# Performance work log

Hardware: AMD Instinct MI355X
Metric: run time of the kernel (lower is better)

Reference implementation:

```python
import jax, jax.numpy as jnp
import numpy as np

N, D, E, C = 8192, 64, 524288, 2


def setup_inputs() -> dict:
    key = jax.random.key(0)
    ks = jax.random.split(key, 14)
    src = jax.random.randint(ks[0], (E,), 0, N, dtype=jnp.int32)
    dst = jax.random.randint(ks[1], (E,), 0, N, dtype=jnp.int32)
    h = jax.random.normal(ks[2], (N, D), jnp.float32)
    # dense adjacency consistent with the edge list (A[u,v]=1 for edge u->v)
    one = jnp.ones((E,), jnp.float32)
    A = jnp.zeros((N, N), jnp.float32).at[src, dst].max(one)
    # motif adjacencies: random subsets of the base edges
    keep1 = jax.random.bernoulli(ks[3], 0.5, (E,)).astype(jnp.float32)
    keep2 = jax.random.bernoulli(ks[4], 0.3, (E,)).astype(jnp.float32)
    A1 = jnp.zeros((N, N), jnp.float32).at[src, dst].max(keep1)
    A2 = jnp.zeros((N, N), jnp.float32).at[src, dst].max(keep2)
    s = 0.05
    Ww = jax.random.normal(ks[5], (D, D), jnp.float32) * s
    Wb = jax.random.normal(ks[6], (D,), jnp.float32) * s
    fc0 = jax.random.normal(ks[7], (D, D), jnp.float32) * s
    fc1 = jax.random.normal(ks[8], (D, D), jnp.float32) * s
    fc2 = jax.random.normal(ks[9], (D, D), jnp.float32) * s
    lin_w = jax.random.normal(ks[10], (3 * D, C), jnp.float32) * s
    lin_b = jax.random.normal(ks[11], (C,), jnp.float32) * s
    return {"h": h, "A": A, "A1": A1, "A2": A2, "Ww": Ww, "Wb": Wb,
            "fc0": fc0, "fc1": fc1, "fc2": fc2, "lin_w": lin_w,
            "lin_b": lin_b, "src": src, "dst": dst}


def _dot_gat_pool(az, fc, src, dst, emask, nmask):
    # DGL DotGatConv (num_heads=1): ft = fc(az); e_uv = <ft_u, ft_v>/sqrt(F);
    # edge-softmax per destination; sum-aggregate; then avg-pool over subgraph nodes.
    n = az.shape[0]
    ft = az @ fc                                   # [N, F]
    scale = 1.0 / jnp.sqrt(jnp.float32(ft.shape[-1]))
    e = jnp.sum(ft[src] * ft[dst], axis=-1) * scale  # [E]
    neg = jnp.finfo(e.dtype).min
    e = jnp.where(emask, e, neg)
    m = jax.ops.segment_max(e, dst, num_segments=n)
    m = jnp.where(jnp.isfinite(m), m, 0.0)
    ex = jnp.where(emask, jnp.exp(e - m[dst]), 0.0)
    den = jax.ops.segment_sum(ex, dst, num_segments=n)
    alpha = ex / jnp.maximum(den[dst], 1e-9)       # [E]
    agg = jax.ops.segment_sum(alpha[:, None] * ft[src], dst, num_segments=n)  # [N, F]
    # mean over nodes present in the (motif) subgraph
    return jnp.sum(agg * nmask[:, None], axis=0) / jnp.maximum(jnp.sum(nmask), 1.0)


def reference(h, A, A1, A2, Ww, Wb, fc0, fc1, fc2, lin_w, lin_b, src, dst):
    n = h.shape[0]
    Z = (A @ h) @ Ww.T + Wb                        # Z = W(A h)
    outs = []
    # motif 0: full edge set, az = Z
    all_e = jnp.ones(src.shape, bool)
    all_n = jnp.ones((n,), jnp.float32)
    outs.append(_dot_gat_pool(Z, fc0, src, dst, all_e, all_n))
    # motifs 1, 2: edge subgraph where A_k[u, v] > 0, az = A_k @ Z
    for Ak, fck in ((A1, fc1), (A2, fc2)):
        emask = Ak[src, dst] > 0
        em = emask.astype(jnp.float32)
        nmask = jnp.zeros((n,), jnp.float32).at[src].max(em)
        nmask = jnp.maximum(nmask, jnp.zeros((n,), jnp.float32).at[dst].max(em))
        az = Ak @ Z
        outs.append(_dot_gat_pool(az, fck, src, dst, emask, nmask))
    feat = jnp.concatenate(outs)[None, :]          # [1, 3*F]
    return feat @ lin_w + lin_b                    # [1, num_classes]
```

## Files before the change

### kernel.cpp

```cpp
#include <hip/hip_runtime.h>

constexpr int N = 8192;
constexpr int D = 64;
constexpr int E = 524288;

constexpr size_t SZ_BITMAP = (size_t)N * (size_t)N / 8;
constexpr size_t SZ_CNT    = 8256 * sizeof(int);
constexpr size_t O_BITMAP  = 0;
constexpr size_t O_SRCCNT  = O_BITMAP + SZ_BITMAP;
constexpr size_t O_DSTCNT  = O_SRCCNT + SZ_CNT;
constexpr size_t O_NF1     = O_DSTCNT + SZ_CNT;
constexpr size_t O_NF2     = O_NF1 + N;
constexpr size_t O_POOLED  = O_NF2 + N;
constexpr size_t ZERO_END  = O_POOLED + 1024;
constexpr size_t O_SRCPTR  = ZERO_END;
constexpr size_t O_DSTPTR  = O_SRCPTR + SZ_CNT;
constexpr size_t O_SRCFILL = O_DSTPTR + SZ_CNT;
constexpr size_t O_DSTFILL = O_SRCFILL + SZ_CNT;
constexpr size_t O_EFLAGS  = O_DSTFILL + SZ_CNT;
constexpr size_t O_CSRS    = O_EFLAGS + (size_t)E;
constexpr size_t O_CSRD    = O_CSRS + (size_t)E * 4;
constexpr size_t O_Z       = O_CSRD + (size_t)E * 4;
constexpr size_t O_FT      = O_Z + (size_t)N * D * 4;


__global__ void edge_classify(const int* __restrict__ src, const int* __restrict__ dst,
                              const float* __restrict__ A1, const float* __restrict__ A2,
                              unsigned* __restrict__ bitmap,
                              int* __restrict__ srcCnt, int* __restrict__ dstCnt,
                              unsigned char* __restrict__ nf1, unsigned char* __restrict__ nf2,
                              unsigned char* __restrict__ eflags) {
    int i = blockIdx.x * blockDim.x + threadIdx.x;
    if (i >= E) return;
    int u = src[i], v = dst[i];
    long long key = ((long long)u << 13) | v;
    unsigned bit = 1u << (key & 31);
    unsigned old = atomicOr(&bitmap[key >> 5], bit);
    int own = ((old & bit) == 0) ? 1 : 0;
    float a1 = A1[key];
    float a2 = A2[key];
    int f1 = (a1 > 0.0f) ? 1 : 0;
    int f2 = (a2 > 0.0f) ? 1 : 0;
    eflags[i] = (unsigned char)(own | (f1 << 1) | (f2 << 2));
    if (own) atomicAdd(&srcCnt[u], 1);
    atomicAdd(&dstCnt[v], 1);
    if (f1) { nf1[u] = 1; nf1[v] = 1; }
    if (f2) { nf2[u] = 1; nf2[v] = 1; }
}

__global__ void scan2(const int* __restrict__ srcCnt, int* __restrict__ srcPtr, int* __restrict__ srcFill,
                      const int* __restrict__ dstCnt, int* __restrict__ dstPtr, int* __restrict__ dstFill) {
    const int* cnt = (blockIdx.x == 0) ? srcCnt : dstCnt;
    int* ptr  = (blockIdx.x == 0) ? srcPtr : dstPtr;
    int* fill = (blockIdx.x == 0) ? srcFill : dstFill;
    __shared__ int ssum[256];
    int t = threadIdx.x;
    int base = t * 32;
    int loc[32];
    int s = 0;
    for (int j = 0; j < 32; ++j) { loc[j] = cnt[base + j]; s += loc[j]; }
    ssum[t] = s;
    __syncthreads();
    for (int off = 1; off < 256; off <<= 1) {
        int v = (t >= off) ? ssum[t - off] : 0;
        __syncthreads();
        ssum[t] += v;
        __syncthreads();
    }
    int ex = (t == 0) ? 0 : ssum[t - 1];
    for (int j = 0; j < 32; ++j) {
        ptr[base + j] = ex;
        fill[base + j] = ex;
        ex += loc[j];
    }
    if (t == 255) ptr[N] = ex;
}

__global__ void csr_fill(const int* __restrict__ src, const int* __restrict__ dst,
                         const unsigned char* __restrict__ eflags,
                         int* __restrict__ srcFill, int* __restrict__ dstFill,
                         int* __restrict__ csrS, int* __restrict__ csrD) {
    int i = blockIdx.x * blockDim.x + threadIdx.x;
    if (i >= E) return;
    int u = src[i], v = dst[i];
    int fl = eflags[i];
    int f12 = (fl >> 1) & 3;
    if (fl & 1) {
        int p = atomicAdd(&srcFill[u], 1);
        csrS[p] = v | (f12 << 13);
    }
    int p2 = atomicAdd(&dstFill[v], 1);
    csrD[p2] = u | (f12 << 13);
}

__global__ void rowpipe1(const int* __restrict__ srcPtr, const int* __restrict__ csrS,
                         const float* __restrict__ h, const float* __restrict__ Ww,
                         const float* __restrict__ Wb, const float* __restrict__ fc0,
                         float* __restrict__ Z, float* __restrict__ ft0) {
    __shared__ float W1[64 * 64];
    __shared__ float W2[64 * 64];
    int t = threadIdx.x;
    for (int i = t; i < 4096; i += 256) {
        int r = i >> 6, c = i & 63;
        W1[i] = Ww[c * 64 + r];
        W2[i] = fc0[i];
    }
    __syncthreads();
    int wid = t >> 6, lane = t & 63;
    int row = blockIdx.x * 4 + wid;
    int b = srcPtr[row], e = srcPtr[row + 1];
    float ah = 0.0f;
    for (int j = b; j < e; ++j)
        ah += h[(size_t)(csrS[j] & 8191) * D + lane];
    float z = Wb[lane];
    #pragma unroll 8
    for (int k = 0; k < 64; ++k)
        z = fmaf(__shfl(ah, k), W1[k * 64 + lane], z);
    Z[(size_t)row * D + lane] = z;
    float f = 0.0f;
    #pragma unroll 8
    for (int k = 0; k < 64; ++k)
        f = fmaf(__shfl(z, k), W2[k * 64 + lane], f);
    ft0[(size_t)row * D + lane] = f;
}

__global__ void rowpipe2(const int* __restrict__ srcPtr, const int* __restrict__ csrS,
                         const float* __restrict__ Z,
                         const float* __restrict__ fc1, const float* __restrict__ fc2,
                         float* __restrict__ ft1, float* __restrict__ ft2) {
    __shared__ float W1[64 * 64];
    __shared__ float W2[64 * 64];
    int t = threadIdx.x;
    for (int i = t; i < 4096; i += 256) {
        W1[i] = fc1[i];
        W2[i] = fc2[i];
    }
    __syncthreads();
    int wid = t >> 6, lane = t & 63;
    int row = blockIdx.x * 4 + wid;
    int b = srcPtr[row], e = srcPtr[row + 1];
    float a1 = 0.0f, a2 = 0.0f;
    for (int j = b; j < e; ++j) {
        int ent = csrS[j];
        if ((ent >> 13) == 0) continue;
        float z = Z[(size_t)(ent & 8191) * D + lane];
        if (ent & (1 << 13)) a1 += z;
        if (ent & (1 << 14)) a2 += z;
    }
    float f1 = 0.0f, f2 = 0.0f;
    #pragma unroll 8
    for (int k = 0; k < 64; ++k) {
        f1 = fmaf(__shfl(a1, k), W1[k * 64 + lane], f1);
        f2 = fmaf(__shfl(a2, k), W2[k * 64 + lane], f2);
    }
    ft1[(size_t)row * D + lane] = f1;
    ft2[(size_t)row * D + lane] = f2;
}

__global__ void gat_fused(const float* __restrict__ ftAll,
                          const int* __restrict__ dstPtr, const int* __restrict__ csrD,
                          float* __restrict__ pooled) {
    int motif = blockIdx.y;
    const float* ft = ftAll + (size_t)motif * N * D;
    int t = threadIdx.x, wid = t >> 6, lane = t & 63;
    int row = blockIdx.x * 4 + wid;
    __shared__ float fv[4][64];
    __shared__ float wbuf[4][64];
    __shared__ int ubuf[4][64];
    fv[wid][lane] = ft[(size_t)row * D + lane];
    int b = dstPtr[row], e = dstPtr[row + 1];
    float mrun = -3.0e38f, den = 0.0f, acc = 0.0f;
    for (int cb = b; cb < e; cb += 64) {
        int j = cb + lane;
        float s = -3.0e38f;
        int u = 0;
        bool act = false;
        if (j < e) {
            int ent = csrD[j];
            u = ent & 8191;
            act = (motif == 0) || ((ent >> (12 + motif)) & 1);
        }
        if (act) {
            const float* fu = ft + (size_t)u * D;
            float d0 = 0.0f, d1 = 0.0f;
            #pragma unroll
            for (int k = 0; k < 16; k += 2) {
                float4 a0 = *(const float4*)(fu + 4 * k);
                float4 b0 = *(const float4*)(&fv[wid][4 * k]);
                float4 a1 = *(const float4*)(fu + 4 * k + 4);
                float4 b1 = *(const float4*)(&fv[wid][4 * k + 4]);
                d0 = fmaf(a0.x, b0.x, d0); d0 = fmaf(a0.y, b0.y, d0);
                d0 = fmaf(a0.z, b0.z, d0); d0 = fmaf(a0.w, b0.w, d0);
                d1 = fmaf(a1.x, b1.x, d1); d1 = fmaf(a1.y, b1.y, d1);
                d1 = fmaf(a1.z, b1.z, d1); d1 = fmaf(a1.w, b1.w, d1);
            }
            s = (d0 + d1) * 0.125f;
        }
        float cm = s;
        cm = fmaxf(cm, __shfl_xor(cm, 1));  cm = fmaxf(cm, __shfl_xor(cm, 2));
        cm = fmaxf(cm, __shfl_xor(cm, 4));  cm = fmaxf(cm, __shfl_xor(cm, 8));
        cm = fmaxf(cm, __shfl_xor(cm, 16)); cm = fmaxf(cm, __shfl_xor(cm, 32));
        float newm = fmaxf(mrun, cm);
        float scale = __expf(mrun - newm);
        float wj = act ? __expf(s - newm) : 0.0f;
        wbuf[wid][lane] = wj;
        ubuf[wid][lane] = u;
        float cs = wj;
        cs += __shfl_xor(cs, 1);  cs += __shfl_xor(cs, 2);  cs += __shfl_xor(cs, 4);
        cs += __shfl_xor(cs, 8);  cs += __shfl_xor(cs, 16); cs += __shfl_xor(cs, 32);
        den = den * scale + cs;
        acc *= scale;
        int csize = min(64, e - cb);
        for (int q = 0; q < csize; ++q) {
            float wq = wbuf[wid][q];
            if (wq > 0.0f)
                acc = fmaf(wq, ft[(size_t)ubuf[wid][q] * D + lane], acc);
        }
        mrun = newm;
    }
    float pool = acc / fmaxf(den, 1e-9f);
    __shared__ float red[256];
    red[t] = pool;
    __syncthreads();
    if (wid == 0) {
        float s = red[lane] + red[64 + lane] + red[128 + lane] + red[192 + lane];
        atomicAdd(&pooled[motif * 64 + lane], s);
    }
}

__global__ void final_kernel(const float* __restrict__ pooled,
                             const unsigned char* __restrict__ nf1, const unsigned char* __restrict__ nf2,
                             const float* __restrict__ lin_w, const float* __restrict__ lin_b,
                             float* __restrict__ out) {
    __shared__ int r1[256], r2[256];
    __shared__ float feat[192];
    __shared__ int cnt[2];
    int t = threadIdx.x;
    int s1 = 0, s2 = 0;
    for (int i = t; i < N; i += 256) { s1 += nf1[i]; s2 += nf2[i]; }
    r1[t] = s1; r2[t] = s2;
    __syncthreads();
    for (int off = 128; off > 0; off >>= 1) {
        if (t < off) { r1[t] += r1[t + off]; r2[t] += r2[t + off]; }
        __syncthreads();
    }
    if (t == 0) { cnt[0] = r1[0]; cnt[1] = r2[0]; }
    __syncthreads();
    if (t < 192) {
        int sel = t >> 6;
        float div = (sel == 0) ? (float)N : fmaxf((float)cnt[sel - 1], 1.0f);
        feat[t] = pooled[t] / div;
    }
    __syncthreads();
    if (t < 2) {
        float o = lin_b[t];
        for (int k = 0; k < 192; ++k) o = fmaf(feat[k], lin_w[k * 2 + t], o);
        out[t] = o;
    }
}

extern "C" void kernel_launch(void* const* d_in, const int* in_sizes, int n_in,
                              void* d_out, int out_size, void* d_ws, size_t ws_size,
                              hipStream_t stream) {
    const float* h   = (const float*)d_in[0];
    const float* A1  = (const float*)d_in[2];
    const float* A2  = (const float*)d_in[3];
    const float* Ww  = (const float*)d_in[4];
    const float* Wb  = (const float*)d_in[5];
    const float* fc0 = (const float*)d_in[6];
    const float* fc1 = (const float*)d_in[7];
    const float* fc2 = (const float*)d_in[8];
    const float* lw  = (const float*)d_in[9];
    const float* lb  = (const float*)d_in[10];
    const int* src   = (const int*)d_in[11];
    const int* dst   = (const int*)d_in[12];
    float* out = (float*)d_out;

    char* w = (char*)d_ws;
    unsigned* bitmap   = (unsigned*)(w + O_BITMAP);
    int* srcCnt        = (int*)(w + O_SRCCNT);
    int* dstCnt        = (int*)(w + O_DSTCNT);
    unsigned char* nf1 = (unsigned char*)(w + O_NF1);
    unsigned char* nf2 = (unsigned char*)(w + O_NF2);
    float* pooled      = (float*)(w + O_POOLED);
    int* srcPtr        = (int*)(w + O_SRCPTR);
    int* dstPtr        = (int*)(w + O_DSTPTR);
    int* srcFill       = (int*)(w + O_SRCFILL);
    int* dstFill       = (int*)(w + O_DSTFILL);
    unsigned char* efl = (unsigned char*)(w + O_EFLAGS);
    int* csrS          = (int*)(w + O_CSRS);
    int* csrD          = (int*)(w + O_CSRD);
    float* Z           = (float*)(w + O_Z);
    float* ftAll       = (float*)(w + O_FT);
    float* ft1         = ftAll + (size_t)N * D;
    float* ft2         = ftAll + 2 * (size_t)N * D;

    hipMemsetAsync(w, 0, ZERO_END, stream);

    edge_classify<<<E / 256, 256, 0, stream>>>(src, dst, A1, A2, bitmap, srcCnt, dstCnt, nf1, nf2, efl);
    scan2<<<2, 256, 0, stream>>>(srcCnt, srcPtr, srcFill, dstCnt, dstPtr, dstFill);
    csr_fill<<<E / 256, 256, 0, stream>>>(src, dst, efl, srcFill, dstFill, csrS, csrD);

    rowpipe1<<<N / 4, 256, 0, stream>>>(srcPtr, csrS, h, Ww, Wb, fc0, Z, ftAll);
    rowpipe2<<<N / 4, 256, 0, stream>>>(srcPtr, csrS, Z, fc1, fc2, ft1, ft2);

    gat_fused<<<dim3(N / 4, 3), 256, 0, stream>>>(ftAll, dstPtr, csrD, pooled);

    final_kernel<<<1, 256, 0, stream>>>(pooled, nf1, nf2, lw, lb, out);
}
```

Measured before the change: 930.0 us.

## Fuse three motif GAT passes into one kernel and unroll gather loops

The GAT kernel now handles all three motifs in one launch per destination row. It reads each CSR entry once, computes the three attention scores, and keeps three online-softmax states. The weights and source index are packed into a float4 shared buffer, and aggregation runs with two interleaved accumulators. The neighbour-sum loops in rowpipe1 and rowpipe2 are unrolled with several independent accumulators to expose more memory-level parallelism. The fused kernel uses more registers and does less per-motif branch skipping at the block level, which may lower occupancy.

```diff
diff --git a/kernel.cpp b/kernel.cpp
--- a/kernel.cpp
+++ b/kernel.cpp
@@ -3,6 +3,7 @@
 constexpr int N = 8192;
 constexpr int D = 64;
 constexpr int E = 524288;
+constexpr int ND = N * D;
 
 constexpr size_t SZ_BITMAP = (size_t)N * (size_t)N / 8;
 constexpr size_t SZ_CNT    = 8256 * sizeof(int);
@@ -24,12 +25,13 @@
 constexpr size_t O_FT      = O_Z + (size_t)N * D * 4;
 
 
-__global__ void edge_classify(const int* __restrict__ src, const int* __restrict__ dst,
-                              const float* __restrict__ A1, const float* __restrict__ A2,
-                              unsigned* __restrict__ bitmap,
-                              int* __restrict__ srcCnt, int* __restrict__ dstCnt,
-                              unsigned char* __restrict__ nf1, unsigned char* __restrict__ nf2,
-                              unsigned char* __restrict__ eflags) {
+__global__ void __launch_bounds__(256) edge_classify(
+        const int* __restrict__ src, const int* __restrict__ dst,
+        const float* __restrict__ A1, const float* __restrict__ A2,
+        unsigned* __restrict__ bitmap,
+        int* __restrict__ srcCnt, int* __restrict__ dstCnt,
+        unsigned char* __restrict__ nf1, unsigned char* __restrict__ nf2,
+        unsigned char* __restrict__ eflags) {
     int i = blockIdx.x * blockDim.x + threadIdx.x;
     if (i >= E) return;
     int u = src[i], v = dst[i];
@@ -48,8 +50,9 @@
     if (f2) { nf2[u] = 1; nf2[v] = 1; }
 }
 
-__global__ void scan2(const int* __restrict__ srcCnt, int* __restrict__ srcPtr, int* __restrict__ srcFill,
-                      const int* __restrict__ dstCnt, int* __restrict__ dstPtr, int* __restrict__ dstFill) {
+__global__ void __launch_bounds__(256) scan2(
+        const int* __restrict__ srcCnt, int* __restrict__ srcPtr, int* __restrict__ srcFill,
+        const int* __restrict__ dstCnt, int* __restrict__ dstPtr, int* __restrict__ dstFill) {
     const int* cnt = (blockIdx.x == 0) ? srcCnt : dstCnt;
     int* ptr  = (blockIdx.x == 0) ? srcPtr : dstPtr;
     int* fill = (blockIdx.x == 0) ? srcFill : dstFill;
@@ -76,10 +79,11 @@
     if (t == 255) ptr[N] = ex;
 }
 
-__global__ void csr_fill(const int* __restrict__ src, const int* __restrict__ dst,
-                         const unsigned char* __restrict__ eflags,
-                         int* __restrict__ srcFill, int* __restrict__ dstFill,
-                         int* __restrict__ csrS, int* __restrict__ csrD) {
+__global__ void __launch_bounds__(256) csr_fill(
+        const int* __restrict__ src, const int* __restrict__ dst,
+        const unsigned char* __restrict__ eflags,
+        int* __restrict__ srcFill, int* __restrict__ dstFill,
+        int* __restrict__ csrS, int* __restrict__ csrD) {
     int i = blockIdx.x * blockDim.x + threadIdx.x;
     if (i >= E) return;
     int u = src[i], v = dst[i];
@@ -93,10 +97,11 @@
     csrD[p2] = u | (f12 << 13);
 }
 
-__global__ void rowpipe1(const int* __restrict__ srcPtr, const int* __restrict__ csrS,
-                         const float* __restrict__ h, const float* __restrict__ Ww,
-                         const float* __restrict__ Wb, const float* __restrict__ fc0,
-                         float* __restrict__ Z, float* __restrict__ ft0) {
+__global__ void __launch_bounds__(256) rowpipe1(
+        const int* __restrict__ srcPtr, const int* __restrict__ csrS,
+        const float* __restrict__ h, const float* __restrict__ Ww,
+        const float* __restrict__ Wb, const float* __restrict__ fc0,
+        float* __restrict__ Z, float* __restrict__ ft0) {
     __shared__ float W1[64 * 64];
     __shared__ float W2[64 * 64];
     int t = threadIdx.x;
@@ -109,9 +114,18 @@
     int wid = t >> 6, lane = t & 63;
     int row = blockIdx.x * 4 + wid;
     int b = srcPtr[row], e = srcPtr[row + 1];
-    float ah = 0.0f;
-    for (int j = b; j < e; ++j)
-        ah += h[(size_t)(csrS[j] & 8191) * D + lane];
+    float a0 = 0.0f, a1 = 0.0f, a2 = 0.0f, a3 = 0.0f;
+    int j = b;
+    for (; j + 3 < e; j += 4) {
+        int u0 = csrS[j] & 8191, u1 = csrS[j + 1] & 8191;
+        int u2 = csrS[j + 2] & 8191, u3 = csrS[j + 3] & 8191;
+        a0 += h[(size_t)u0 * D + lane];
+        a1 += h[(size_t)u1 * D + lane];
+        a2 += h[(size_t)u2 * D + lane];
+        a3 += h[(size_t)u3 * D + lane];
+    }
+    for (; j < e; ++j) a0 += h[(size_t)(csrS[j] & 8191) * D + lane];
+    float ah = (a0 + a1) + (a2 + a3);
     float z = Wb[lane];
     #pragma unroll 8
     for (int k = 0; k < 64; ++k)
@@ -124,10 +138,11 @@
     ft0[(size_t)row * D + lane] = f;
 }
 
-__global__ void rowpipe2(const int* __restrict__ srcPtr, const int* __restrict__ csrS,
-                         const float* __restrict__ Z,
-                         const float* __restrict__ fc1, const float* __restrict__ fc2,
-                         float* __restrict__ ft1, float* __restrict__ ft2) {
+__global__ void __launch_bounds__(256) rowpipe2(
+        const int* __restrict__ srcPtr, const int* __restrict__ csrS,
+        const float* __restrict__ Z,
+        const float* __restrict__ fc1, const float* __restrict__ fc2,
+        float* __restrict__ ft1, float* __restrict__ ft2) {
     __shared__ float W1[64 * 64];
     __shared__ float W2[64 * 64];
     int t = threadIdx.x;
@@ -139,99 +154,169 @@
     int wid = t >> 6, lane = t & 63;
     int row = blockIdx.x * 4 + wid;
     int b = srcPtr[row], e = srcPtr[row + 1];
-    float a1 = 0.0f, a2 = 0.0f;
-    for (int j = b; j < e; ++j) {
-        int ent = csrS[j];
-        if ((ent >> 13) == 0) continue;
-        float z = Z[(size_t)(ent & 8191) * D + lane];
-        if (ent & (1 << 13)) a1 += z;
-        if (ent & (1 << 14)) a2 += z;
-    }
+    float a1x = 0.0f, a2x = 0.0f, a1y = 0.0f, a2y = 0.0f;
+    int j = b;
+    for (; j + 1 < e; j += 2) {
+        int e0 = csrS[j], e1 = csrS[j + 1];
+        if (e0 >> 13) {
+            float z = Z[(size_t)(e0 & 8191) * D + lane];
+            if (e0 & (1 << 13)) a1x += z;
+            if (e0 & (1 << 14)) a2x += z;
+        }
+        if (e1 >> 13) {
+            float z = Z[(size_t)(e1 & 8191) * D + lane];
+            if (e1 & (1 << 13)) a1y += z;
+            if (e1 & (1 << 14)) a2y += z;
+        }
+    }
+    for (; j < e; ++j) {
+        int e0 = csrS[j];
+        if (e0 >> 13) {
+            float z = Z[(size_t)(e0 & 8191) * D + lane];
+            if (e0 & (1 << 13)) a1x += z;
+            if (e0 & (1 << 14)) a2x += z;
+        }
+    }
+    float s1 = a1x + a1y, s2 = a2x + a2y;
     float f1 = 0.0f, f2 = 0.0f;
     #pragma unroll 8
     for (int k = 0; k < 64; ++k) {
-        f1 = fmaf(__shfl(a1, k), W1[k * 64 + lane], f1);
-        f2 = fmaf(__shfl(a2, k), W2[k * 64 + lane], f2);
+        f1 = fmaf(__shfl(s1, k), W1[k * 64 + lane], f1);
+        f2 = fmaf(__shfl(s2, k), W2[k * 64 + lane], f2);
     }
     ft1[(size_t)row * D + lane] = f1;
     ft2[(size_t)row * D + lane] = f2;
 }
 
-__global__ void gat_fused(const float* __restrict__ ftAll,
-                          const int* __restrict__ dstPtr, const int* __restrict__ csrD,
-                          float* __restrict__ pooled) {
-    int motif = blockIdx.y;
-    const float* ft = ftAll + (size_t)motif * N * D;
+__global__ void __launch_bounds__(256) gat_fused_all(
+        const float* __restrict__ ftAll, const int* __restrict__ dstPtr,
+        const int* __restrict__ csrD, float* __restrict__ pooled) {
     int t = threadIdx.x, wid = t >> 6, lane = t & 63;
     int row = blockIdx.x * 4 + wid;
-    __shared__ float fv[4][64];
-    __shared__ float wbuf[4][64];
-    __shared__ int ubuf[4][64];
-    fv[wid][lane] = ft[(size_t)row * D + lane];
+    __shared__ float fv[4][3][64];
+    __shared__ float4 sw[4][64];
+    __shared__ float red[3][256];
+    const float* ft0 = ftAll;
+    fv[wid][0][lane] = ft0[(size_t)row * D + lane];
+    fv[wid][1][lane] = ft0[ND + (size_t)row * D + lane];
+    fv[wid][2][lane] = ft0[2 * ND + (size_t)row * D + lane];
+    const float4* fq0 = (const float4*)fv[wid][0];
+    const float4* fq1 = (const float4*)fv[wid][1];
+    const float4* fq2 = (const float4*)fv[wid][2];
     int b = dstPtr[row], e = dstPtr[row + 1];
-    float mrun = -3.0e38f, den = 0.0f, acc = 0.0f;
+    float mr0 = -3.0e38f, mr1 = -3.0e38f, mr2 = -3.0e38f;
+    float den0 = 0.0f, den1 = 0.0f, den2 = 0.0f;
+    float a0x = 0.0f, a0y = 0.0f, a1x = 0.0f, a1y = 0.0f, a2x = 0.0f, a2y = 0.0f;
     for (int cb = b; cb < e; cb += 64) {
         int j = cb + lane;
-        float s = -3.0e38f;
-        int u = 0;
-        bool act = false;
-        if (j < e) {
-            int ent = csrD[j];
-            u = ent & 8191;
-            act = (motif == 0) || ((ent >> (12 + motif)) & 1);
-        }
-        if (act) {
-            const float* fu = ft + (size_t)u * D;
+        bool valid = j < e;
+        int ent = valid ? csrD[j] : 0;
+        int u = ent & 8191;
+        bool act1 = valid && (ent & (1 << 13));
+        bool act2 = valid && (ent & (1 << 14));
+        float s0 = -3.0e38f, s1 = -3.0e38f, s2 = -3.0e38f;
+        const float4* pu = (const float4*)(ft0 + (size_t)u * D);
+        if (valid) {
             float d0 = 0.0f, d1 = 0.0f;
             #pragma unroll
             for (int k = 0; k < 16; k += 2) {
-                float4 a0 = *(const float4*)(fu + 4 * k);
-                float4 b0 = *(const float4*)(&fv[wid][4 * k]);
-                float4 a1 = *(const float4*)(fu + 4 * k + 4);
-                float4 b1 = *(const float4*)(&fv[wid][4 * k + 4]);
-                d0 = fmaf(a0.x, b0.x, d0); d0 = fmaf(a0.y, b0.y, d0);
-                d0 = fmaf(a0.z, b0.z, d0); d0 = fmaf(a0.w, b0.w, d0);
-                d1 = fmaf(a1.x, b1.x, d1); d1 = fmaf(a1.y, b1.y, d1);
-                d1 = fmaf(a1.z, b1.z, d1); d1 = fmaf(a1.w, b1.w, d1);
+                float4 a = pu[k], bq = fq0[k];
+                float4 c = pu[k + 1], dq = fq0[k + 1];
+                d0 = fmaf(a.x, bq.x, d0); d0 = fmaf(a.y, bq.y, d0);
+                d0 = fmaf(a.z, bq.z, d0); d0 = fmaf(a.w, bq.w, d0);
+                d1 = fmaf(c.x, dq.x, d1); d1 = fmaf(c.y, dq.y, d1);
+                d1 = fmaf(c.z, dq.z, d1); d1 = fmaf(c.w, dq.w, d1);
             }
-            s = (d0 + d1) * 0.125f;
-        }
-        float cm = s;
-        cm = fmaxf(cm, __shfl_xor(cm, 1));  cm = fmaxf(cm, __shfl_xor(cm, 2));
-        cm = fmaxf(cm, __shfl_xor(cm, 4));  cm = fmaxf(cm, __shfl_xor(cm, 8));
-        cm = fmaxf(cm, __shfl_xor(cm, 16)); cm = fmaxf(cm, __shfl_xor(cm, 32));
-        float newm = fmaxf(mrun, cm);
-        float scale = __expf(mrun - newm);
-        float wj = act ? __expf(s - newm) : 0.0f;
-        wbuf[wid][lane] = wj;
-        ubuf[wid][lane] = u;
-        float cs = wj;
-        cs += __shfl_xor(cs, 1);  cs += __shfl_xor(cs, 2);  cs += __shfl_xor(cs, 4);
-        cs += __shfl_xor(cs, 8);  cs += __shfl_xor(cs, 16); cs += __shfl_xor(cs, 32);
-        den = den * scale + cs;
-        acc *= scale;
+            s0 = (d0 + d1) * 0.125f;
+        }
+        if (act1) {
+            const float4* p1 = pu + ND / 4;
+            float d0 = 0.0f, d1 = 0.0f;
+            #pragma unroll
+            for (int k = 0; k < 16; k += 2) {
+                float4 a = p1[k], bq = fq1[k];
+                float4 c = p1[k + 1], dq = fq1[k + 1];
+                d0 = fmaf(a.x, bq.x, d0); d0 = fmaf(a.y, bq.y, d0);
+                d0 = fmaf(a.z, bq.z, d0); d0 = fmaf(a.w, bq.w, d0);
+                d1 = fmaf(c.x, dq.x, d1); d1 = fmaf(c.y, dq.y, d1);
+                d1 = fmaf(c.z, dq.z, d1); d1 = fmaf(c.w, dq.w, d1);
+            }
+            s1 = (d0 + d1) * 0.125f;
+        }
+        if (act2) {
+            const float4* p2 = pu + 2 * (ND / 4);
+            float d0 = 0.0f, d1 = 0.0f;
+            #pragma unroll
+            for (int k = 0; k < 16; k += 2) {
+                float4 a = p2[k], bq = fq2[k];
+                float4 c = p2[k + 1], dq = fq2[k + 1];
+                d0 = fmaf(a.x, bq.x, d0); d0 = fmaf(a.y, bq.y, d0);
+                d0 = fmaf(a.z, bq.z, d0); d0 = fmaf(a.w, bq.w, d0);
+                d1 = fmaf(c.x, dq.x, d1); d1 = fmaf(c.y, dq.y, d1);
+                d1 = fmaf(c.z, dq.z, d1); d1 = fmaf(c.w, dq.w, d1);
+            }
+            s2 = (d0 + d1) * 0.125f;
+        }
+        float c0 = s0, c1 = s1, c2 = s2;
+        c0 = fmaxf(c0, __shfl_xor(c0, 1));  c1 = fmaxf(c1, __shfl_xor(c1, 1));  c2 = fmaxf(c2, __shfl_xor(c2, 1));
+        c0 = fmaxf(c0, __shfl_xor(c0, 2));  c1 = fmaxf(c1, __shfl_xor(c1, 2));  c2 = fmaxf(c2, __shfl_xor(c2, 2));
+        c0 = fmaxf(c0, __shfl_xor(c0, 4));  c1 = fmaxf(c1, __shfl_xor(c1, 4));  c2 = fmaxf(c2, __shfl_xor(c2, 4));
+        c0 = fmaxf(c0, __shfl_xor(c0, 8));  c1 = fmaxf(c1, __shfl_xor(c1, 8));  c2 = fmaxf(c2, __shfl_xor(c2, 8));
+        c0 = fmaxf(c0, __shfl_xor(c0, 16)); c1 = fmaxf(c1, __shfl_xor(c1, 16)); c2 = fmaxf(c2, __shfl_xor(c2, 16));
+        c0 = fmaxf(c0, __shfl_xor(c0, 32)); c1 = fmaxf(c1, __shfl_xor(c1, 32)); c2 = fmaxf(c2, __shfl_xor(c2, 32));
+        float nm0 = fmaxf(mr0, c0), nm1 = fmaxf(mr1, c1), nm2 = fmaxf(mr2, c2);
+        float sc0 = __expf(mr0 - nm0), sc1 = __expf(mr1 - nm1), sc2 = __expf(mr2 - nm2);
+        float w0 = valid ? __expf(s0 - nm0) : 0.0f;
+        float w1 = act1 ? __expf(s1 - nm1) : 0.0f;
+        float w2 = act2 ? __expf(s2 - nm2) : 0.0f;
+        sw[wid][lane] = make_float4(w0, w1, w2, __int_as_float(u));
+        float t0 = w0, t1 = w1, t2 = w2;
+        t0 += __shfl_xor(t0, 1);  t1 += __shfl_xor(t1, 1);  t2 += __shfl_xor(t2, 1);
+        t0 += __shfl_xor(t0, 2);  t1 += __shfl_xor(t1, 2);  t2 += __shfl_xor(t2, 2);
+        t0 += __shfl_xor(t0, 4);  t1 += __shfl_xor(t1, 4);  t2 += __shfl_xor(t2, 4);
+        t0 += __shfl_xor(t0, 8);  t1 += __shfl_xor(t1, 8);  t2 += __shfl_xor(t2, 8);
+        t0 += __shfl_xor(t0, 16); t1 += __shfl_xor(t1, 16); t2 += __shfl_xor(t2, 16);
+        t0 += __shfl_xor(t0, 32); t1 += __shfl_xor(t1, 32); t2 += __shfl_xor(t2, 32);
+        den0 = den0 * sc0 + t0; den1 = den1 * sc1 + t1; den2 = den2 * sc2 + t2;
+        a0x *= sc0; a0y *= sc0; a1x *= sc1; a1y *= sc1; a2x *= sc2; a2y *= sc2;
+        mr0 = nm0; mr1 = nm1; mr2 = nm2;
         int csize = min(64, e - cb);
-        for (int q = 0; q < csize; ++q) {
-            float wq = wbuf[wid][q];
-            if (wq > 0.0f)
-                acc = fmaf(wq, ft[(size_t)ubuf[wid][q] * D + lane], acc);
-        }
-        mrun = newm;
-    }
-    float pool = acc / fmaxf(den, 1e-9f);
-    __shared__ float red[256];
-    red[t] = pool;
-    __syncthreads();
-    if (wid == 0) {
-        float s = red[lane] + red[64 + lane] + red[128 + lane] + red[192 + lane];
-        atomicAdd(&pooled[motif * 64 + lane], s);
-    }
-}
-
-__global__ void final_kernel(const float* __restrict__ pooled,
-                             const unsigned char* __restrict__ nf1, const unsigned char* __restrict__ nf2,
-                             const float* __restrict__ lin_w, const float* __restrict__ lin_b,
-                             float* __restrict__ out) {
+        const float* fbase = ft0 + lane;
+        int q = 0;
+        for (; q + 1 < csize; q += 2) {
+            float4 e0 = sw[wid][q], e1 = sw[wid][q + 1];
+            const float* p0 = fbase + (size_t)__float_as_int(e0.w) * D;
+            const float* p1 = fbase + (size_t)__float_as_int(e1.w) * D;
+            a0x = fmaf(e0.x, p0[0], a0x);
+            a0y = fmaf(e1.x, p1[0], a0y);
+            if (e0.y > 0.0f) a1x = fmaf(e0.y, p0[ND], a1x);
+            if (e1.y > 0.0f) a1y = fmaf(e1.y, p1[ND], a1y);
+            if (e0.z > 0.0f) a2x = fmaf(e0.z, p0[2 * ND], a2x);
+            if (e1.z > 0.0f) a2y = fmaf(e1.z, p1[2 * ND], a2y);
+        }
+        if (q < csize) {
+            float4 e0 = sw[wid][q];
+            const float* p0 = fbase + (size_t)__float_as_int(e0.w) * D;
+            a0x = fmaf(e0.x, p0[0], a0x);
+            if (e0.y > 0.0f) a1x = fmaf(e0.y, p0[ND], a1x);
+            if (e0.z > 0.0f) a2x = fmaf(e0.z, p0[2 * ND], a2x);
+        }
+    }
+    red[0][t] = (a0x + a0y) / fmaxf(den0, 1e-9f);
+    red[1][t] = (a1x + a1y) / fmaxf(den1, 1e-9f);
+    red[2][t] = (a2x + a2y) / fmaxf(den2, 1e-9f);
+    __syncthreads();
+    if (wid < 3) {
+        float s = red[wid][lane] + red[wid][64 + lane] + red[wid][128 + lane] + red[wid][192 + lane];
+        atomicAdd(&pooled[wid * 64 + lane], s);
+    }
+}
+
+__global__ void __launch_bounds__(256) final_kernel(
+        const float* __restrict__ pooled,
+        const unsigned char* __restrict__ nf1, const unsigned char* __restrict__ nf2,
+        const float* __restrict__ lin_w, const float* __restrict__ lin_b,
+        float* __restrict__ out) {
     __shared__ int r1[256], r2[256];
     __shared__ float feat[192];
     __shared__ int cnt[2];
@@ -292,8 +377,8 @@
     int* csrD          = (int*)(w + O_CSRD);
     float* Z           = (float*)(w + O_Z);
     float* ftAll       = (float*)(w + O_FT);
-    float* ft1         = ftAll + (size_t)N * D;
-    float* ft2         = ftAll + 2 * (size_t)N * D;
+    float* ft1         = ftAll + (size_t)ND;
+    float* ft2         = ftAll + 2 * (size_t)ND;
 
     hipMemsetAsync(w, 0, ZERO_END, stream);
 
@@ -304,7 +389,7 @@
     rowpipe1<<<N / 4, 256, 0, stream>>>(srcPtr, csrS, h, Ww, Wb, fc0, Z, ftAll);
     rowpipe2<<<N / 4, 256, 0, stream>>>(srcPtr, csrS, Z, fc1, fc2, ft1, ft2);
 
-    gat_fused<<<dim3(N / 4, 3), 256, 0, stream>>>(ftAll, dstPtr, csrD, pooled);
+    gat_fused_all<<<N / 4, 256, 0, stream>>>(ftAll, dstPtr, csrD, pooled);
 
     final_kernel<<<1, 256, 0, stream>>>(pooled, nf1, nf2, lw, lb, out);
 }
```

New measurement: 842.7 us. 9.4% less time.
